# Optimization experiments

Hardware: AMD Instinct MI355X
Metric: run time of the kernel (lower is better)

## Reference

```python
import jax, jax.numpy as jnp
import numpy as np

B, N, C = 8, 4096, 768
H, HD = 12, 64          # num_heads, head_dim = C // H
M = HD * 2              # rand_feat_dim
LAM = 0.3
NUM_STEP = 5


def setup_inputs() -> dict:
    key = jax.random.key(0)
    k1, k2, k3, k4 = jax.random.split(key, 4)
    x = jax.random.normal(k1, (B, N, C), dtype=jnp.float32)
    Wqkv = jax.random.normal(k2, (C, 2 * C), dtype=jnp.float32) * 0.02
    Wproj = jax.random.normal(k3, (C, C), dtype=jnp.float32) * 0.02
    bproj = jnp.zeros((C,), dtype=jnp.float32)
    rand_matrix = jax.random.normal(k4, (H, HD, M), dtype=jnp.float32)
    return {"x": x, "Wqkv": Wqkv, "Wproj": Wproj, "bproj": bproj,
            "rand_matrix": rand_matrix}


def _soft(z, t):
    # sign(z) * relu(|z| - t): soft-thresholding (ISTA proximal step)
    return jnp.sign(z) * jax.nn.relu(jnp.abs(z) - t)


def reference(x, Wqkv, Wproj, bproj, rand_matrix):
    Bn, Nn, Cn = x.shape
    Hh, hd, m = rand_matrix.shape
    scale = hd ** (-0.5)

    qkv = x @ Wqkv                                   # [B,N,2C]
    q = qkv[..., :Cn].reshape(Bn, Nn, Hh, hd).transpose(0, 2, 1, 3)  # [B,H,N,hd]
    v = qkv[..., Cn:].reshape(Bn, Nn, Hh, hd).transpose(0, 2, 1, 3)  # [B,H,N,hd]

    # random-feature map: exp(q @ proj - ||q||^2 / 2) / sqrt(m)
    qs = q * scale ** 0.5
    rf = jnp.exp(jnp.einsum('bhnd,hdm->bhnm', qs, rand_matrix)
                 - 0.5 * jnp.sum(qs * qs, axis=-1, keepdims=True)) / m ** 0.5
    # F.normalize(p=2, dim=-2): normalize over the sequence axis
    qn = rf / jnp.maximum(jnp.linalg.norm(rf, axis=-2, keepdims=True), 1e-12)

    kk = jnp.einsum('bhnm,bhnp->bhmp', qn, qn)       # [B,H,m,m]
    kv = jnp.einsum('bhnm,bhnd->bhmd', qn, v)        # [B,H,m,hd]

    # Lipschitz bound: max row L1 norm of kk, detached
    L = jax.lax.stop_gradient(
        jnp.max(jnp.sum(jnp.abs(kk), axis=-1), axis=-1))[..., None, None] + 1.0

    # unrolled ISTA soft-thresholding loop
    s = _soft(kv, LAM)
    for _ in range(NUM_STEP):
        s = _soft(s - (kk @ s - kv) / L, LAM / L)

    out = jnp.einsum('bhnm,bhmd->bhnd', qn, s)       # [B,H,N,hd]
    out = out.transpose(0, 2, 1, 3).reshape(Bn, Nn, Cn)
    return out @ Wproj + bproj
```

## Files before the change

### kernel.cpp

```cpp
#include <hip/hip_runtime.h>


typedef __attribute__((ext_vector_type(8))) short bf16x8;
typedef __attribute__((ext_vector_type(4))) float f32x4;

#define GLD16(gptr, lptr)                                                              \
  __builtin_amdgcn_global_load_lds((const __attribute__((address_space(1))) void*)(gptr), \
                                   (__attribute__((address_space(3))) void*)(lptr), 16, 0, 0)

__device__ __forceinline__ unsigned short f2bf(float f) {
  union { float f; unsigned int u; } v; v.f = f;
  unsigned int r = v.u + 0x7fffu + ((v.u >> 16) & 1u);
  return (unsigned short)(r >> 16);
}
__device__ __forceinline__ float bf2f(unsigned short s) {
  union { unsigned int u; float f; } v; v.u = ((unsigned int)s) << 16;
  return v.f;
}
__device__ __forceinline__ float rn_of(float css) {
  return 1.f / fmaxf(sqrtf(css), 1e-12f);
}

template<int KT>
__device__ __forceinline__ void gemm256_core(
    const unsigned short* __restrict__ A,
    const unsigned short* __restrict__ B,
    int ldk,
    f32x4 (&acc)[8][4],
    unsigned short* smem) {
  const int tid = threadIdx.x;
  const int lane = tid & 63, wave = tid >> 6;
  const int l16 = lane & 15, quad = lane >> 4;
  const int wr = wave >> 2, wc = wave & 3;
  const int fsw = (l16 >> 1) & 3;
  const int r0 = tid >> 2;
  const int gsw = (((tid & 3) ^ ((r0 >> 1) & 3)) << 3);

#pragma unroll
  for (int i = 0; i < 8; i++)
#pragma unroll
    for (int j = 0; j < 4; j++)
#pragma unroll
      for (int r = 0; r < 4; r++) acc[i][j][r] = 0.f;

  const unsigned short* Ag0 = A + (long)r0 * ldk + gsw;
  const unsigned short* Ag1 = A + (long)(r0 + 128) * ldk + gsw;
  const unsigned short* Bg0 = B + (long)r0 * ldk + gsw;
  const unsigned short* Bg1 = B + (long)(r0 + 128) * ldk + gsw;
  const int ldsW = wave * 64 * 8;

  auto stage = [&](int t, int b) {
    unsigned short* Ab = smem + b * 16384;
    unsigned short* Bb = Ab + 8192;
    const int k0 = t * 32;
    GLD16(Ag0 + k0, Ab + ldsW);
    GLD16(Ag1 + k0, Ab + 4096 + ldsW);
    GLD16(Bg0 + k0, Bb + ldsW);
    GLD16(Bg1 + k0, Bb + 4096 + ldsW);
  };

  stage(0, 0);
  stage(1, 1);
  asm volatile("s_waitcnt vmcnt(4)" ::: "memory");
  __builtin_amdgcn_s_barrier();

  for (int t = 0; t < KT; t++) {
    const int b = t & 1;
    const unsigned short* Ab = smem + b * 16384;
    const unsigned short* Bb = Ab + 8192;
    bf16x8 af[8], bf[4];
#pragma unroll
    for (int i = 0; i < 8; i++)
      af[i] = *(const bf16x8*)(Ab + (wr * 128 + i * 16 + l16) * 32 + ((quad ^ fsw) * 8));
#pragma unroll
    for (int j = 0; j < 4; j++)
      bf[j] = *(const bf16x8*)(Bb + (wc * 64 + j * 16 + l16) * 32 + ((quad ^ fsw) * 8));
    asm volatile("s_waitcnt lgkmcnt(0)" ::: "memory");
    __builtin_amdgcn_s_barrier();
    __builtin_amdgcn_s_setprio(1);
#pragma unroll
    for (int i = 0; i < 8; i++)
#pragma unroll
      for (int j = 0; j < 2; j++)
        acc[i][j] = __builtin_amdgcn_mfma_f32_16x16x32_bf16(af[i], bf[j], acc[i][j], 0, 0, 0);
    __builtin_amdgcn_s_setprio(0);
    asm volatile("" ::: "memory");
    __builtin_amdgcn_s_barrier();
    if (t + 2 < KT) stage(t + 2, b);
    asm volatile("" ::: "memory");
    __builtin_amdgcn_s_barrier();
    __builtin_amdgcn_s_setprio(1);
#pragma unroll
    for (int i = 0; i < 8; i++)
#pragma unroll
      for (int j = 2; j < 4; j++)
        acc[i][j] = __builtin_amdgcn_mfma_f32_16x16x32_bf16(af[i], bf[j], acc[i][j], 0, 0, 0);
    __builtin_amdgcn_s_setprio(0);
    if (t + 2 < KT) {
      asm volatile("s_waitcnt vmcnt(4)" ::: "memory");
    } else {
      asm volatile("s_waitcnt vmcnt(0)" ::: "memory");
    }
    __builtin_amdgcn_s_barrier();
  }
}

template<int BM, int BN>
__device__ __forceinline__ void gemm_core_nt(
    const unsigned short* __restrict__ A, int lda,
    const unsigned short* __restrict__ B0,
    const unsigned short* __restrict__ B1, int brows0, int ldb,
    int K,
    f32x4 (&acc)[BM / 32][BN / 32],
    unsigned short* As, unsigned short* Bs) {
  constexpr int MT = BM / 32, NT = BN / 32;
  const int tid = threadIdx.x;
  const int lane = tid & 63, wave = tid >> 6;
  const int wm = (wave >> 1) * (BM / 2), wn = (wave & 1) * (BN / 2);
  const int l16 = lane & 15, quad = lane >> 4;
  const int arow = tid >> 2;
  const int akos = (((tid & 3) ^ ((arow >> 1) & 3)) << 3);
  const int fsw = (l16 >> 1) & 3;
#pragma unroll
  for (int i = 0; i < MT; i++)
#pragma unroll
    for (int j = 0; j < NT; j++)
#pragma unroll
      for (int r = 0; r < 4; r++) acc[i][j][r] = 0.f;

  for (int k0 = 0; k0 < K; k0 += 32) {
    __syncthreads();
#pragma unroll
    for (int c = 0; c < BM / 64; c++) {
      const unsigned short* gp = A + (long)(arow + c * 64) * lda + k0 + akos;
      GLD16(gp, As + (c * 256 + wave * 64) * 8);
    }
#pragma unroll
    for (int c = 0; c < BN / 64; c++) {
      int row = arow + c * 64;
      const unsigned short* bp = (row < brows0) ? (B0 + (long)row * ldb)
                                                : (B1 + (long)(row - brows0) * ldb);
      GLD16(bp + k0 + akos, Bs + (c * 256 + wave * 64) * 8);
    }
    __syncthreads();
    bf16x8 af[MT], bfr[NT];
#pragma unroll
    for (int i = 0; i < MT; i++)
      af[i] = *(const bf16x8*)(As + (wm + i * 16 + l16) * 32 + ((quad ^ fsw) * 8));
#pragma unroll
    for (int j = 0; j < NT; j++)
      bfr[j] = *(const bf16x8*)(Bs + (wn + j * 16 + l16) * 32 + ((quad ^ fsw) * 8));
#pragma unroll
    for (int i = 0; i < MT; i++)
#pragma unroll
      for (int j = 0; j < NT; j++)
        acc[i][j] = __builtin_amdgcn_mfma_f32_16x16x32_bf16(af[i], bfr[j], acc[i][j], 0, 0, 0);
  }
}

__global__ __launch_bounds__(256) void k_convert_bf16(const float* __restrict__ in,
                                                      unsigned short* __restrict__ out, long n4) {
  long i = (long)blockIdx.x * 256 + threadIdx.x;
  if (i < n4) {
    float4 v = ((const float4*)in)[i];
    unsigned short o[4] = {f2bf(v.x), f2bf(v.y), f2bf(v.z), f2bf(v.w)};
    ((uint2*)out)[i] = *(uint2*)o;
  }
}

__global__ __launch_bounds__(256) void k_transpose_tiled(const float* __restrict__ in,
                                                         unsigned short* __restrict__ out,
                                                         int R, int C, float scale) {
  __shared__ float t[32][33];
  const float* ib = in + (long)blockIdx.z * R * C;
  unsigned short* ob = out + (long)blockIdx.z * R * C;
  int c0 = blockIdx.x * 32, r0 = blockIdx.y * 32;
  int tx = threadIdx.x & 31, ty = threadIdx.x >> 5;
#pragma unroll
  for (int k = 0; k < 32; k += 8)
    t[ty + k][tx] = ib[(long)(r0 + ty + k) * C + c0 + tx];
  __syncthreads();
#pragma unroll
  for (int k = 0; k < 32; k += 8)
    ob[(long)(c0 + ty + k) * R + r0 + tx] = f2bf(t[tx][ty + k] * scale);
}

__global__ __launch_bounds__(512, 2) void k_gemm_qkv256(const unsigned short* __restrict__ xbf,
                                                        const unsigned short* __restrict__ wqkvT,
                                                        unsigned short* __restrict__ q,
                                                        unsigned short* __restrict__ vT) {
  __shared__ __align__(16) unsigned short smem[36864];
  f32x4 acc[8][4];
  const int L = blockIdx.x;
  const int xcd = L & 7, slot = L >> 3;
  const int rt = xcd * 16 + slot / 6;
  const int ct = slot % 6;
  gemm256_core<24>(xbf + (long)rt * 256 * 768, wqkvT + (long)ct * 256 * 768, 768, acc, smem);

  const int tid = threadIdx.x, lane = tid & 63, wave = tid >> 6;
  const int l16 = lane & 15, quad = lane >> 4;
  const int wr = wave >> 2, wc = wave & 3;
  const int b = rt >> 4;
  const int nbase = (rt & 15) * 256;
  if (ct < 3) {
#pragma unroll
    for (int i = 0; i < 8; i++)
#pragma unroll
      for (int j = 0; j < 4; j++) {
        int col = ct * 256 + wc * 64 + j * 16 + l16;
        int h = col >> 6, d = col & 63;
#pragma unroll
        for (int r = 0; r < 4; r++) {
          int n = nbase + wr * 128 + i * 16 + quad * 4 + r;
          q[((long)(b * 12 + h) * 4096 + n) * 64 + d] = f2bf(acc[i][j][r]);
        }
      }
  } else {
    unsigned short* pool = smem;
    for (int hh = 0; hh < 2; hh++) {
      __syncthreads();
      if (wr == hh) {
#pragma unroll
        for (int i = 0; i < 8; i++)
#pragma unroll
          for (int j = 0; j < 4; j++)
#pragma unroll
            for (int r = 0; r < 4; r++)
              pool[(wc * 64 + j * 16 + l16) * 136 + i * 16 + quad * 4 + r] = f2bf(acc[i][j][r]);
      }
      __syncthreads();
#pragma unroll
      for (int it = 0; it < 8; it++) {
        int chunk = it * 512 + tid;
        int col = chunk >> 4, ng = chunk & 15;
        uint4 val = *(const uint4*)&pool[col * 136 + ng * 8];
        int vcol = (ct - 3) * 256 + col;
        int h = vcol >> 6, d = vcol & 63;
        long n = nbase + hh * 128 + ng * 8;
        *(uint4*)&vT[((long)(b * 12 + h) * 64 + d) * 4096 + n] = val;
      }
    }
  }
}

__global__ __launch_bounds__(256) void k_gemm_rf(const unsigned short* __restrict__ q,
                                                 const unsigned short* __restrict__ rmT,
                                                 unsigned short* __restrict__ qnT,
                                                 float* __restrict__ colss) {
  __shared__ __align__(16) unsigned short smem[16384];
  __shared__ float hnp[256];
  __shared__ float css[128];
  unsigned short* Asm = smem;
  unsigned short* Bsm = smem + 8192;
  unsigned short* pool = smem;
  f32x4 acc[4][4];
  const int nt = blockIdx.x, bh = blockIdx.y, h = bh % 12;
  const int tid = threadIdx.x, lane = tid & 63, wave = tid >> 6;
  const int l16 = lane & 15, quad = lane >> 4;
  const int wm = (wave >> 1) * 64, wn = (wave & 1) * 64;
  const int fsw = (l16 >> 1) & 3;
  const unsigned short* Aq = q + ((long)bh * 4096 + nt * 128) * 64;
  const unsigned short* Brm = rmT + (long)h * 8192;

#pragma unroll
  for (int c = 0; c < 4; c++) {
    int chunk = c * 256 + tid;
    int row = chunk >> 3, ko8 = chunk & 7;
    int kc = ko8 >> 2;
    int c2s = (ko8 & 3) ^ ((row >> 1) & 3);
    *(uint4*)(Asm + kc * 4096 + row * 32 + c2s * 8) = *(const uint4*)(Aq + (long)row * 64 + ko8 * 8);
    *(uint4*)(Bsm + kc * 4096 + row * 32 + c2s * 8) = *(const uint4*)(Brm + (long)row * 64 + ko8 * 8);
  }
  for (int i = tid; i < 128; i += 256) css[i] = 0.f;
  __syncthreads();
  {
    const unsigned short* ap = Asm + (tid & 1) * 4096 + (tid >> 1) * 32;
    float ssum = 0.f;
#pragma unroll
    for (int e = 0; e < 32; e++) { float f = bf2f(ap[e]); ssum += f * f; }
    hnp[tid] = ssum;
  }
#pragma unroll
  for (int i = 0; i < 4; i++)
#pragma unroll
    for (int j = 0; j < 4; j++)
#pragma unroll
      for (int r = 0; r < 4; r++) acc[i][j][r] = 0.f;
#pragma unroll
  for (int kc = 0; kc < 2; kc++) {
    bf16x8 af[4], bfr[4];
#pragma unroll
    for (int i = 0; i < 4; i++)
      af[i] = *(const bf16x8*)(Asm + kc * 4096 + (wm + i * 16 + l16) * 32 + ((quad ^ fsw) * 8));
#pragma unroll
    for (int j = 0; j < 4; j++)
      bfr[j] = *(const bf16x8*)(Bsm + kc * 4096 + (wn + j * 16 + l16) * 32 + ((quad ^ fsw) * 8));
#pragma unroll
    for (int i = 0; i < 4; i++)
#pragma unroll
      for (int j = 0; j < 4; j++)
        acc[i][j] = __builtin_amdgcn_mfma_f32_16x16x32_bf16(af[i], bfr[j], acc[i][j], 0, 0, 0);
  }
  __syncthreads();
  float hnv[4][4];
#pragma unroll
  for (int i = 0; i < 4; i++)
#pragma unroll
    for (int r = 0; r < 4; r++) {
      int row = wm + i * 16 + quad * 4 + r;
      hnv[i][r] = 0.0625f * (hnp[2 * row] + hnp[2 * row + 1]);
    }
#pragma unroll
  for (int j = 0; j < 4; j++) {
    int col = wn + j * 16 + l16;
    float cp = 0.f;
#pragma unroll
    for (int i = 0; i < 4; i++)
#pragma unroll
      for (int r = 0; r < 4; r++) {
        float v = __expf(acc[i][j][r] - hnv[i][r]) * 0.08838834764831845f;
        acc[i][j][r] = v;
        cp += v * v;
      }
    atomicAdd(&css[col], cp);
  }
  __syncthreads();
  for (int i = tid; i < 128; i += 256) atomicAdd(&colss[bh * 128 + i], css[i]);
  for (int hh = 0; hh < 2; hh++) {
    __syncthreads();
    if ((wave >> 1) == hh) {
#pragma unroll
      for (int i = 0; i < 4; i++)
#pragma unroll
        for (int j = 0; j < 4; j++)
#pragma unroll
          for (int r = 0; r < 4; r++)
            pool[(i * 16 + quad * 4 + r) * 134 + wn + j * 16 + l16] = f2bf(acc[i][j][r]);
    }
    __syncthreads();
#pragma unroll
    for (int c = 0; c < 4; c++) {
      int chunk = tid + c * 256;
      int m = chunk >> 3, nj = (chunk & 7) * 8;
      unsigned short o[8];
#pragma unroll
      for (int e = 0; e < 8; e++) o[e] = pool[(nj + e) * 134 + m];
      *(uint4*)&qnT[((long)bh * 128 + m) * 4096 + nt * 128 + hh * 64 + nj] = *(uint4*)o;
    }
  }
}

__global__ __launch_bounds__(256) void k_gemm_kkkv(const unsigned short* __restrict__ qnT,
                                                   const unsigned short* __restrict__ vT,
                                                   const float* __restrict__ colss,
                                                   unsigned short* __restrict__ kkp) {
  __shared__ __align__(16) unsigned short As[128 * 32], Bs[192 * 32];
  f32x4 acc[4][6];
  const int ks = blockIdx.x, bh = blockIdx.y;
  const unsigned short* A = qnT + (long)bh * 128 * 4096 + ks * 512;
  const unsigned short* B1 = vT + (long)bh * 64 * 4096 + ks * 512;
  gemm_core_nt<128, 192>(A, 4096, A, B1, 128, 4096, 512, acc, As, Bs);
  const int lane = threadIdx.x & 63, wave = threadIdx.x >> 6;
  const int l16 = lane & 15, quad = lane >> 4;
  const int wm = (wave >> 1) * 64, wn = (wave & 1) * 96;
  unsigned short* dst = kkp + ((long)ks * 96 + bh) * 24576;
  float rnr[4][4];
#pragma unroll
  for (int i = 0; i < 4; i++)
#pragma unroll
    for (int r = 0; r < 4; r++)
      rnr[i][r] = rn_of(colss[bh * 128 + wm + i * 16 + quad * 4 + r]);
#pragma unroll
  for (int j = 0; j < 6; j++) {
    int col = wn + j * 16 + l16;
    float rnc = (col < 128) ? rn_of(colss[bh * 128 + col]) : 1.f;
#pragma unroll
    for (int i = 0; i < 4; i++)
#pragma unroll
      for (int r = 0; r < 4; r++) {
        int row = wm + i * 16 + quad * 4 + r;
        dst[row * 192 + col] = f2bf(acc[i][j][r] * rnr[i][r] * rnc);
      }
  }
}

__global__ __launch_bounds__(256) void k_ista(const unsigned short* __restrict__ kkp,
                                              const float* __restrict__ colss,
                                              unsigned short* __restrict__ sT) {
  __shared__ __align__(16) unsigned short kks[128 * 144];
  __shared__ __align__(16) unsigned short ssT[64 * 144];
  __shared__ float kvs[128 * 64];
  __shared__ float red[128];
  __shared__ float rns[128];
  const int tid = threadIdx.x, lane = tid & 63, wave = tid >> 6;
  const int l16 = lane & 15, quad = lane >> 4;
  const int wm = (wave >> 1) * 64, wn = (wave & 1) * 32;
  const int bh = blockIdx.x;
  const unsigned short* base = kkp + (long)bh * 24576;
  for (int idx = tid; idx < 3072; idx += 256) {
    int m = idx / 24, c8 = idx % 24;
    float f[8] = {0.f, 0.f, 0.f, 0.f, 0.f, 0.f, 0.f, 0.f};
#pragma unroll
    for (int ks = 0; ks < 8; ks++) {
      union { uint4 u; unsigned short s[8]; } u;
      u.u = *(const uint4*)(base + (long)ks * 2359296 + m * 192 + c8 * 8);
#pragma unroll
      for (int e = 0; e < 8; e++) f[e] += bf2f(u.s[e]);
    }
    if (c8 < 16) {
#pragma unroll
      for (int e = 0; e < 8; e++) kks[m * 144 + c8 * 8 + e] = f2bf(f[e]);
    } else {
#pragma unroll
      for (int e = 0; e < 8; e++) kvs[m * 64 + (c8 - 16) * 8 + e] = f[e];
    }
  }
  __syncthreads();
  float kv[4][2][4];
#pragma unroll
  for (int i = 0; i < 4; i++)
#pragma unroll
    for (int j = 0; j < 2; j++)
#pragma unroll
      for (int r = 0; r < 4; r++) {
        int m = wm + i * 16 + quad * 4 + r, d = wn + j * 16 + l16;
        kv[i][j][r] = kvs[m * 64 + d];
      }
  if (tid < 128) {
    float rs = 0.f;
    const unsigned short* rp = kks + tid * 144;
    for (int p = 0; p < 128; p++) rs += fabsf(bf2f(rp[p]));
    red[tid] = rs;
    rns[tid] = rn_of(colss[bh * 128 + tid]);
  }
  __syncthreads();
  for (int o = 64; o > 0; o >>= 1) {
    if (tid < o) red[tid] = fmaxf(red[tid], red[tid + o]);
    __syncthreads();
  }
  const float L = red[0] + 1.f;
  const float invL = 1.f / L;
  const float lamL = 0.3f * invL;
  float sreg[4][2][4];
#pragma unroll
  for (int i = 0; i < 4; i++)
#pragma unroll
    for (int j = 0; j < 2; j++)
#pragma unroll
      for (int r = 0; r < 4; r++) {
        float z = kv[i][j][r];
        float az = fabsf(z) - 0.3f;
        float s = az > 0.f ? copysignf(az, z) : 0.f;
        sreg[i][j][r] = s;
        ssT[(wn + j * 16 + l16) * 144 + wm + i * 16 + quad * 4 + r] = f2bf(s);
      }
  for (int step = 0; step < 5; step++) {
    __syncthreads();
    f32x4 acc[4][2];
#pragma unroll
    for (int i = 0; i < 4; i++)
#pragma unroll
      for (int j = 0; j < 2; j++)
#pragma unroll
        for (int r = 0; r < 4; r++) acc[i][j][r] = 0.f;
#pragma unroll
    for (int kc = 0; kc < 4; kc++) {
      bf16x8 af[4], bfj[2];
#pragma unroll
      for (int i = 0; i < 4; i++)
        af[i] = *(const bf16x8*)(kks + (wm + i * 16 + l16) * 144 + kc * 32 + quad * 8);
#pragma unroll
      for (int j = 0; j < 2; j++)
        bfj[j] = *(const bf16x8*)(ssT + (wn + j * 16 + l16) * 144 + kc * 32 + quad * 8);
#pragma unroll
      for (int i = 0; i < 4; i++)
#pragma unroll
        for (int j = 0; j < 2; j++)
          acc[i][j] = __builtin_amdgcn_mfma_f32_16x16x32_bf16(af[i], bfj[j], acc[i][j], 0, 0, 0);
    }
    __syncthreads();
#pragma unroll
    for (int i = 0; i < 4; i++)
#pragma unroll
      for (int j = 0; j < 2; j++)
#pragma unroll
        for (int r = 0; r < 4; r++) {
          float z = sreg[i][j][r] - (acc[i][j][r] - kv[i][j][r]) * invL;
          float az = fabsf(z) - lamL;
          float s = az > 0.f ? copysignf(az, z) : 0.f;
          sreg[i][j][r] = s;
          ssT[(wn + j * 16 + l16) * 144 + wm + i * 16 + quad * 4 + r] = f2bf(s);
        }
  }
#pragma unroll
  for (int i = 0; i < 4; i++)
#pragma unroll
    for (int j = 0; j < 2; j++)
#pragma unroll
      for (int r = 0; r < 4; r++) {
        int m = wm + i * 16 + quad * 4 + r, d = wn + j * 16 + l16;
        sT[(long)bh * 8192 + d * 128 + m] = f2bf(sreg[i][j][r] * rns[m]);
      }
}

__global__ __launch_bounds__(256) void k_gemm_attn(const unsigned short* __restrict__ qnT,
                                                   const unsigned short* __restrict__ sT,
                                                   unsigned short* __restrict__ attn) {
  __shared__ __align__(16) unsigned short As2[32 * 128];
  __shared__ __align__(16) unsigned short Bs[64 * 32];
  f32x4 acc[4][2];
  const int nt = blockIdx.x, bh = blockIdx.y;
  const int b = bh / 12, h = bh % 12;
  const int tid = threadIdx.x, lane = tid & 63, wave = tid >> 6;
  const int l16 = lane & 15, quad = lane >> 4;
  const int wm = (wave >> 1) * 64, wn = (wave & 1) * 32;
  const int fsw = (l16 >> 1) & 3;
#pragma unroll
  for (int i = 0; i < 4; i++)
#pragma unroll
    for (int j = 0; j < 2; j++)
#pragma unroll
      for (int r = 0; r < 4; r++) acc[i][j][r] = 0.f;
  for (int k0 = 0; k0 < 128; k0 += 32) {
    __syncthreads();
#pragma unroll
    for (int c = 0; c < 2; c++) {
      int chunk = tid + c * 256;
      int kr = chunk >> 4, n0 = (chunk & 15) * 8;
      const unsigned short* gp = qnT + ((long)bh * 128 + k0 + kr) * 4096 + nt * 128 + n0;
      GLD16(gp, As2 + (c * 256 + wave * 64) * 8);
    }
    {
      int dd = tid >> 2;
      int ko = (((tid & 3) ^ ((dd >> 1) & 3)) * 8);
      const unsigned short* gp = sT + ((long)bh * 64 + dd) * 128 + k0 + ko;
      GLD16(gp, Bs + wave * 512);
    }
    __syncthreads();
    bf16x8 af[4], bfr[2];
#pragma unroll
    for (int i = 0; i < 4; i++) {
      union { bf16x8 v; unsigned short s[8]; } u;
#pragma unroll
      for (int e = 0; e < 8; e++) u.s[e] = As2[(quad * 8 + e) * 128 + wm + i * 16 + l16];
      af[i] = u.v;
    }
#pragma unroll
    for (int j = 0; j < 2; j++)
      bfr[j] = *(const bf16x8*)&Bs[(wn + j * 16 + l16) * 32 + ((quad ^ fsw) * 8)];
#pragma unroll
    for (int i = 0; i < 4; i++)
#pragma unroll
      for (int j = 0; j < 2; j++)
        acc[i][j] = __builtin_amdgcn_mfma_f32_16x16x32_bf16(af[i], bfr[j], acc[i][j], 0, 0, 0);
  }
#pragma unroll
  for (int i = 0; i < 4; i++)
#pragma unroll
    for (int j = 0; j < 2; j++)
#pragma unroll
      for (int r = 0; r < 4; r++) {
        int n = nt * 128 + wm + i * 16 + quad * 4 + r;
        int dd = wn + j * 16 + l16;
        attn[((long)b * 4096 + n) * 768 + h * 64 + dd] = f2bf(acc[i][j][r]);
      }
}

__global__ __launch_bounds__(512, 2) void k_gemm_proj256(const unsigned short* __restrict__ attn,
                                                         const unsigned short* __restrict__ wprojT,
                                                         const float* __restrict__ bias,
                                                         float* __restrict__ out) {
  __shared__ __align__(16) unsigned short smem[32768];
  f32x4 acc[8][4];
  const int L = blockIdx.x;
  const int xcd = L & 7, slot = L >> 3;
  const int rt = xcd * 16 + slot / 3;
  const int ct = slot % 3;
  gemm256_core<24>(attn + (long)rt * 256 * 768, wprojT + (long)ct * 256 * 768, 768, acc, smem);
  const int tid = threadIdx.x, lane = tid & 63, wave = tid >> 6;
  const int l16 = lane & 15, quad = lane >> 4;
  const int wr = wave >> 2, wc = wave & 3;
  const long row0 = (long)rt * 256 + wr * 128;
#pragma unroll
  for (int i = 0; i < 8; i++)
#pragma unroll
    for (int j = 0; j < 4; j++) {
      int col = ct * 256 + wc * 64 + j * 16 + l16;
      float bv = bias[col];
#pragma unroll
      for (int r = 0; r < 4; r++) {
        long row = row0 + i * 16 + quad * 4 + r;
        out[row * 768 + col] = acc[i][j][r] + bv;
      }
    }
}

extern "C" void kernel_launch(void* const* d_in, const int* in_sizes, int n_in,
                              void* d_out, int out_size, void* d_ws, size_t ws_size,
                              hipStream_t stream) {
  const float* x = (const float*)d_in[0];
  const float* Wqkv = (const float*)d_in[1];
  const float* Wproj = (const float*)d_in[2];
  const float* bproj = (const float*)d_in[3];
  const float* rm = (const float*)d_in[4];
  float* out = (float*)d_out;

  size_t o = 0;
  char* wsb = (char*)d_ws;
  auto take = [&](size_t b) { char* p = wsb + o; o += b; return p; };
  unsigned short* wqkvT = (unsigned short*)take(2359296);
  unsigned short* wprojT = (unsigned short*)take(1179648);
  unsigned short* rmT = (unsigned short*)take(196608);
  unsigned short* q = (unsigned short*)take(50331648);
  unsigned short* vT = (unsigned short*)take(50331648);
  float* colss = (float*)take(49152);
  unsigned short* sT = (unsigned short*)take(1572864);
  if (ws_size < o) return;

  unsigned short* xbf = (unsigned short*)d_out;
  unsigned short* qnT = (unsigned short*)d_out;
  unsigned short* kkp = q;
  unsigned short* attnbf = q;

  hipMemsetAsync(colss, 0, 49152, stream);

  k_convert_bf16<<<24576, 256, 0, stream>>>(x, xbf, 6291456L);
  k_transpose_tiled<<<dim3(48, 24, 1), 256, 0, stream>>>(Wqkv, wqkvT, 768, 1536, 1.0f);
  k_transpose_tiled<<<dim3(24, 24, 1), 256, 0, stream>>>(Wproj, wprojT, 768, 768, 1.0f);
  k_transpose_tiled<<<dim3(4, 2, 12), 256, 0, stream>>>(rm, rmT, 64, 128, 0.3535533905932738f);
  k_gemm_qkv256<<<768, 512, 0, stream>>>(xbf, wqkvT, q, vT);
  k_gemm_rf<<<dim3(32, 96), 256, 0, stream>>>(q, rmT, qnT, colss);
  k_gemm_kkkv<<<dim3(8, 96), 256, 0, stream>>>(qnT, vT, colss, kkp);
  k_ista<<<96, 256, 0, stream>>>(kkp, colss, sT);
  k_gemm_attn<<<dim3(32, 96), 256, 0, stream>>>(qnT, sT, attnbf);
  k_gemm_proj256<<<1536 / 4, 512, 0, stream>>>(attnbf, wprojT, bproj, out);
}
```

Measured before the change: 472.3 us.

## Restructure 256x256 GEMM core into 8-phase pipeline with 64-wide K tiles

The shared 256x256 bf16 GEMM core used by the QKV and projection kernels now stages 64-wide K tiles instead of 32-wide ones. The main loop is split into eight fine-grained phases, each issuing a quarter-tile global-to-LDS load, reading A/B fragments, and running a subtile of MFMAs between barriers. LDS use grows to 128 KB per block, with a new 8-way XOR swizzle on the wider rows. The aim is better overlap of global loads, LDS reads and MFMA work with fewer iterations, at the cost of more barriers and larger shared memory that may lower occupancy (the launch bounds still request 2 blocks per CU).

```diff
diff --git a/kernel.cpp b/kernel.cpp
--- a/kernel.cpp
+++ b/kernel.cpp
@@ -21,7 +21,7 @@
   return 1.f / fmaxf(sqrtf(css), 1e-12f);
 }
 
-template<int KT>
+template<int ITERS>
 __device__ __forceinline__ void gemm256_core(
     const unsigned short* __restrict__ A,
     const unsigned short* __restrict__ B,
@@ -32,9 +32,7 @@
   const int lane = tid & 63, wave = tid >> 6;
   const int l16 = lane & 15, quad = lane >> 4;
   const int wr = wave >> 2, wc = wave & 3;
-  const int fsw = (l16 >> 1) & 3;
-  const int r0 = tid >> 2;
-  const int gsw = (((tid & 3) ^ ((r0 >> 1) & 3)) << 3);
+  const int rsw = l16 & 7;
 
 #pragma unroll
   for (int i = 0; i < 8; i++)
@@ -43,66 +41,114 @@
 #pragma unroll
       for (int r = 0; r < 4; r++) acc[i][j][r] = 0.f;
 
-  const unsigned short* Ag0 = A + (long)r0 * ldk + gsw;
-  const unsigned short* Ag1 = A + (long)(r0 + 128) * ldk + gsw;
-  const unsigned short* Bg0 = B + (long)r0 * ldk + gsw;
-  const unsigned short* Bg1 = B + (long)(r0 + 128) * ldk + gsw;
-  const int ldsW = wave * 64 * 8;
-
-  auto stage = [&](int t, int b) {
-    unsigned short* Ab = smem + b * 16384;
-    unsigned short* Bb = Ab + 8192;
-    const int k0 = t * 32;
-    GLD16(Ag0 + k0, Ab + ldsW);
-    GLD16(Ag1 + k0, Ab + 4096 + ldsW);
-    GLD16(Bg0 + k0, Bb + ldsW);
-    GLD16(Bg1 + k0, Bb + 4096 + ldsW);
+  const int srow0 = tid >> 3, sc0 = ((tid & 7) ^ (srow0 & 7)) << 3;
+  const int srow1 = (tid + 512) >> 3, sc1 = ((tid & 7) ^ (srow1 & 7)) << 3;
+  const int dstw = wave * 512;
+
+  auto stageA = [&](int T, int h) {
+    const unsigned short* g = A + (long)(h * 128) * ldk + T * 64;
+    unsigned short* d = smem + (T & 1) * 32768 + h * 8192 + dstw;
+    GLD16(g + (long)srow0 * ldk + sc0, d);
+    GLD16(g + (long)srow1 * ldk + sc1, d + 4096);
   };
-
-  stage(0, 0);
-  stage(1, 1);
+  auto stageB = [&](int T, int h) {
+    const unsigned short* g = B + (long)(h * 128) * ldk + T * 64;
+    unsigned short* d = smem + (T & 1) * 32768 + 16384 + h * 8192 + dstw;
+    GLD16(g + (long)srow0 * ldk + sc0, d);
+    GLD16(g + (long)srow1 * ldk + sc1, d + 4096);
+  };
+
+  bf16x8 af[4][2], bn0[2][2], bn1[2][2];
+
+  auto rdA = [&](int b, int mh) {
+    const unsigned short* p = smem + b * 32768 + wr * 8192 + (mh * 64 + l16) * 64;
+#pragma unroll
+    for (int ii = 0; ii < 4; ii++)
+#pragma unroll
+      for (int ks = 0; ks < 2; ks++)
+        af[ii][ks] = *(const bf16x8*)(p + ii * 1024 + (((ks * 4 + quad) ^ rsw) << 3));
+  };
+  auto rdB = [&](bf16x8 (&bf)[2][2], int b, int nh) {
+    const unsigned short* p = smem + b * 32768 + 16384 + (wc >> 1) * 8192 +
+                              ((wc & 1) * 64 + nh * 32 + l16) * 64;
+#pragma unroll
+    for (int jj = 0; jj < 2; jj++)
+#pragma unroll
+      for (int ks = 0; ks < 2; ks++)
+        bf[jj][ks] = *(const bf16x8*)(p + jj * 1024 + (((ks * 4 + quad) ^ rsw) << 3));
+  };
+
+  auto mma = [&](bf16x8 (&bf)[2][2], int mh, int nh) {
+    __builtin_amdgcn_s_setprio(1);
+#pragma unroll
+    for (int ks = 0; ks < 2; ks++)
+#pragma unroll
+      for (int ii = 0; ii < 4; ii++)
+#pragma unroll
+        for (int jj = 0; jj < 2; jj++)
+          acc[mh * 4 + ii][nh * 2 + jj] = __builtin_amdgcn_mfma_f32_16x16x32_bf16(
+              af[ii][ks], bf[jj][ks], acc[mh * 4 + ii][nh * 2 + jj], 0, 0, 0);
+    __builtin_amdgcn_s_setprio(0);
+  };
+
+#define FENCE asm volatile("" ::: "memory")
+#define DRAIN                                             \
+  asm volatile("s_waitcnt lgkmcnt(0)" ::: "memory");      \
+  __builtin_amdgcn_sched_barrier(0)
+
+  stageA(0, 0); stageA(0, 1); stageB(0, 0); stageB(0, 1);
+  stageB(1, 0); stageB(1, 1);
   asm volatile("s_waitcnt vmcnt(4)" ::: "memory");
   __builtin_amdgcn_s_barrier();
 
-  for (int t = 0; t < KT; t++) {
-    const int b = t & 1;
-    const unsigned short* Ab = smem + b * 16384;
-    const unsigned short* Bb = Ab + 8192;
-    bf16x8 af[8], bf[4];
-#pragma unroll
-    for (int i = 0; i < 8; i++)
-      af[i] = *(const bf16x8*)(Ab + (wr * 128 + i * 16 + l16) * 32 + ((quad ^ fsw) * 8));
-#pragma unroll
-    for (int j = 0; j < 4; j++)
-      bf[j] = *(const bf16x8*)(Bb + (wc * 64 + j * 16 + l16) * 32 + ((quad ^ fsw) * 8));
-    asm volatile("s_waitcnt lgkmcnt(0)" ::: "memory");
-    __builtin_amdgcn_s_barrier();
-    __builtin_amdgcn_s_setprio(1);
-#pragma unroll
-    for (int i = 0; i < 8; i++)
-#pragma unroll
-      for (int j = 0; j < 2; j++)
-        acc[i][j] = __builtin_amdgcn_mfma_f32_16x16x32_bf16(af[i], bf[j], acc[i][j], 0, 0, 0);
-    __builtin_amdgcn_s_setprio(0);
-    asm volatile("" ::: "memory");
-    __builtin_amdgcn_s_barrier();
-    if (t + 2 < KT) stage(t + 2, b);
-    asm volatile("" ::: "memory");
-    __builtin_amdgcn_s_barrier();
-    __builtin_amdgcn_s_setprio(1);
-#pragma unroll
-    for (int i = 0; i < 8; i++)
-#pragma unroll
-      for (int j = 2; j < 4; j++)
-        acc[i][j] = __builtin_amdgcn_mfma_f32_16x16x32_bf16(af[i], bf[j], acc[i][j], 0, 0, 0);
-    __builtin_amdgcn_s_setprio(0);
-    if (t + 2 < KT) {
-      asm volatile("s_waitcnt vmcnt(4)" ::: "memory");
-    } else {
-      asm volatile("s_waitcnt vmcnt(0)" ::: "memory");
-    }
-    __builtin_amdgcn_s_barrier();
-  }
+#pragma unroll 1
+  for (int i = 0; i < ITERS; i++) {
+    const int u = 2 * i;
+    const bool more = (i < ITERS - 1);
+    stageA(u + 1, 0);
+    rdA(0, 0); rdB(bn0, 0, 0);
+    FENCE; __builtin_amdgcn_s_barrier(); DRAIN;
+    mma(bn0, 0, 0);
+    FENCE; __builtin_amdgcn_s_barrier();
+    stageA(u + 1, 1);
+    rdB(bn1, 0, 1);
+    FENCE; __builtin_amdgcn_s_barrier(); DRAIN;
+    mma(bn1, 0, 1);
+    FENCE; __builtin_amdgcn_s_barrier();
+    if (more) stageB(u + 2, 0);
+    rdA(0, 1);
+    FENCE; __builtin_amdgcn_s_barrier(); DRAIN;
+    mma(bn1, 1, 1);
+    FENCE; __builtin_amdgcn_s_barrier();
+    if (more) stageB(u + 2, 1);
+    FENCE; __builtin_amdgcn_s_barrier(); DRAIN;
+    mma(bn0, 1, 0);
+    if (more) { asm volatile("s_waitcnt vmcnt(4)" ::: "memory"); }
+    else      { asm volatile("s_waitcnt vmcnt(0)" ::: "memory"); }
+    FENCE; __builtin_amdgcn_s_barrier();
+    if (more) stageA(u + 2, 0);
+    rdA(1, 0); rdB(bn0, 1, 0);
+    FENCE; __builtin_amdgcn_s_barrier(); DRAIN;
+    mma(bn0, 0, 0);
+    FENCE; __builtin_amdgcn_s_barrier();
+    if (more) stageA(u + 2, 1);
+    rdB(bn1, 1, 1);
+    FENCE; __builtin_amdgcn_s_barrier(); DRAIN;
+    mma(bn1, 0, 1);
+    FENCE; __builtin_amdgcn_s_barrier();
+    if (more) stageB(u + 3, 0);
+    rdA(1, 1);
+    FENCE; __builtin_amdgcn_s_barrier(); DRAIN;
+    mma(bn1, 1, 1);
+    FENCE; __builtin_amdgcn_s_barrier();
+    if (more) stageB(u + 3, 1);
+    FENCE; __builtin_amdgcn_s_barrier(); DRAIN;
+    mma(bn0, 1, 0);
+    asm volatile("s_waitcnt vmcnt(4)" ::: "memory");
+    FENCE; __builtin_amdgcn_s_barrier();
+  }
+#undef FENCE
+#undef DRAIN
 }
 
 template<int BM, int BN>
@@ -189,13 +235,13 @@
                                                         const unsigned short* __restrict__ wqkvT,
                                                         unsigned short* __restrict__ q,
                                                         unsigned short* __restrict__ vT) {
-  __shared__ __align__(16) unsigned short smem[36864];
+  __shared__ __align__(16) unsigned short smem[65536];
   f32x4 acc[8][4];
   const int L = blockIdx.x;
   const int xcd = L & 7, slot = L >> 3;
   const int rt = xcd * 16 + slot / 6;
   const int ct = slot % 6;
-  gemm256_core<24>(xbf + (long)rt * 256 * 768, wqkvT + (long)ct * 256 * 768, 768, acc, smem);
+  gemm256_core<6>(xbf + (long)rt * 256 * 768, wqkvT + (long)ct * 256 * 768, 768, acc, smem);
 
   const int tid = threadIdx.x, lane = tid & 63, wave = tid >> 6;
   const int l16 = lane & 15, quad = lane >> 4;
@@ -570,13 +616,13 @@
                                                          const unsigned short* __restrict__ wprojT,
                                                          const float* __restrict__ bias,
                                                          float* __restrict__ out) {
-  __shared__ __align__(16) unsigned short smem[32768];
+  __shared__ __align__(16) unsigned short smem[65536];
   f32x4 acc[8][4];
   const int L = blockIdx.x;
   const int xcd = L & 7, slot = L >> 3;
   const int rt = xcd * 16 + slot / 3;
   const int ct = slot % 3;
-  gemm256_core<24>(attn + (long)rt * 256 * 768, wprojT + (long)ct * 256 * 768, 768, acc, smem);
+  gemm256_core<6>(attn + (long)rt * 256 * 768, wprojT + (long)ct * 256 * 768, 768, acc, smem);
   const int tid = threadIdx.x, lane = tid & 63, wave = tid >> 6;
   const int l16 = lane & 15, quad = lane >> 4;
   const int wr = wave >> 2, wc = wave & 3;
@@ -633,5 +679,5 @@
   k_gemm_kkkv<<<dim3(8, 96), 256, 0, stream>>>(qnT, vT, colss, kkp);
   k_ista<<<96, 256, 0, stream>>>(kkp, colss, sT);
   k_gemm_attn<<<dim3(32, 96), 256, 0, stream>>>(qnT, sT, attnbf);
-  k_gemm_proj256<<<1536 / 4, 512, 0, stream>>>(attnbf, wprojT, bproj, out);
-}
+  k_gemm_proj256<<<384, 512, 0, stream>>>(attnbf, wprojT, bproj, out);
+}
```

Result: faster. 452.4 us (-4.2%).
